# Optimization experiments

Hardware: AMD Instinct MI355X
Metric: run time of the kernel (lower is better)

## Reference

```python
import jax, jax.numpy as jnp
import numpy as np

V = 10000          # vocab_size
D = 64             # gnn_hidden_dim
L = 8              # tokens per node/edge
DG = 256           # gpt_hidden_dim
NH = 4             # attention heads
N_NODES = 8192
N_EDGES = 2048
PAD = 0
MASK_ID = 4
SPECIAL = jnp.array([0, 1, 2, 3], dtype=jnp.int32)


def setup_inputs() -> dict:
    key = jax.random.key(0)
    ks = jax.random.split(key, 20)
    node_tokens = jax.random.randint(ks[0], (N_NODES, L), 0, V, dtype=jnp.int32)
    edge_tokens = jax.random.randint(ks[1], (N_EDGES, L), 0, V, dtype=jnp.int32)
    edge_index = jax.random.randint(ks[2], (2, N_EDGES), 0, N_NODES, dtype=jnp.int32)
    mask_rows = jax.random.bernoulli(ks[3], 0.15, (N_EDGES,))

    def rn(k, shp, scale):
        return (jax.random.normal(k, shp, jnp.float32) * scale).astype(jnp.float32)

    FD = L * D  # flattened per-node feature dim = 512
    emb = rn(ks[4], (V, D), 0.02).at[PAD].set(0.0)  # padding_idx row zeroed
    W_msg = rn(ks[5], (FD, FD), FD ** -0.5)
    W_node = rn(ks[6], (FD, FD), FD ** -0.5)
    lc1_w = rn(ks[7], (D, DG), D ** -0.5)
    lc1_b = jnp.zeros((DG,), jnp.float32)
    lc2_w = rn(ks[8], (DG, D), DG ** -0.5)
    lc2_b = jnp.zeros((D,), jnp.float32)
    Wq = rn(ks[9], (DG, DG), DG ** -0.5)
    Wk = rn(ks[10], (DG, DG), DG ** -0.5)
    Wv = rn(ks[11], (DG, DG), DG ** -0.5)
    Wo = rn(ks[12], (DG, DG), DG ** -0.5)
    Wf1 = rn(ks[13], (DG, 4 * DG), DG ** -0.5)
    Wf2 = rn(ks[14], (4 * DG, DG), (4 * DG) ** -0.5)
    return {
        "node_tokens": node_tokens, "edge_tokens": edge_tokens,
        "edge_index": edge_index, "mask_rows": mask_rows,
        "emb": emb, "W_msg": W_msg, "W_node": W_node,
        "lc1_w": lc1_w, "lc1_b": lc1_b, "lc2_w": lc2_w, "lc2_b": lc2_b,
        "Wq": Wq, "Wk": Wk, "Wv": Wv, "Wo": Wo, "Wf1": Wf1, "Wf2": Wf2,
    }


def _transformer(x, Wq, Wk, Wv, Wo, Wf1, Wf2):
    # single attention + FFN block; returns hidden states (text_summary[1])
    B, S, Dm = x.shape
    hd = Dm // NH
    q = (x @ Wq).reshape(B, S, NH, hd)
    k = (x @ Wk).reshape(B, S, NH, hd)
    v = (x @ Wv).reshape(B, S, NH, hd)
    att = jnp.einsum('bqhd,bkhd->bhqk', q, k) / jnp.sqrt(jnp.float32(hd))
    a = jax.nn.softmax(att, axis=-1)
    o = jnp.einsum('bhqk,bkhd->bqhd', a, v).reshape(B, S, Dm) @ Wo
    x = x + o
    x = x + jax.nn.gelu(x @ Wf1) @ Wf2
    return x


def reference(node_tokens, edge_tokens, edge_index, mask_rows,
              emb, W_msg, W_node, lc1_w, lc1_b, lc2_w, lc2_b,
              Wq, Wk, Wv, Wo, Wf1, Wf2):
    # --- MLM-style edge-token masking (mask_label with masked_edge=True) ---
    special_ok = ~jnp.isin(edge_tokens, SPECIAL)        # get_special_tokens_mask
    masked_idx = mask_rows[:, None] & special_ok        # [E, L]
    labels = jnp.where(masked_idx, edge_tokens, -100)
    m_tokens = jnp.where(masked_idx, MASK_ID, edge_tokens)

    # --- per-row embedding lookup (vectorized) + flatten to [N, L*D] ---
    x = emb[node_tokens].reshape(N_NODES, L * D)
    e = emb[m_tokens].reshape(N_EDGES, L * D)

    # --- GNN message passing: edge message + scatter-add to dst nodes ---
    src, dst = edge_index[0], edge_index[1]
    msg = jax.nn.relu(e @ W_msg + x[src])               # [E, L*D]
    agg = jax.ops.segment_sum(msg, dst, num_segments=N_NODES)
    h = jax.nn.relu(x @ W_node + agg)                   # [N, L*D]

    # --- edge-index gather-add: embeddings[src] + embeddings[dst] ---
    eh = h[src] + h[dst]                                # [E, L*D]
    z = eh.reshape(N_EDGES, L, D)

    # --- liner_connection_1 -> transformer -> liner_connection_2 ---
    z = z @ lc1_w + lc1_b                               # [E, L, DG]
    hs = _transformer(z, Wq, Wk, Wv, Wo, Wf1, Wf2)
    y = hs @ lc2_w + lc2_b                              # [E, L, D]

    # --- tied lm_head + softmax ---
    logits = y @ emb.T                                  # [E, L, V]
    probs = jax.nn.softmax(logits, axis=-1)
    return labels, probs
```

## Files before the change

### kernel.cpp

```cpp
#include <hip/hip_runtime.h>
#include <math.h>

#define VOCAB 10000
#define DIM 64
#define LTOK 8
#define DGPT 256
#define NHEAD 4
#define NNODES 8192
#define NEDGES 2048
#define FDIM 512
#define NROWS (NEDGES*LTOK)

__global__ __launch_bounds__(256) void k_mask(const int* __restrict__ etok,
                                              const int* __restrict__ mrows,
                                              float* __restrict__ labels,
                                              int* __restrict__ mtok) {
    int i = blockIdx.x * 256 + threadIdx.x;
    int e = i >> 3;
    int t = etok[i];
    bool m = (mrows[e] != 0) && (t > 3);
    labels[i] = m ? (float)t : -100.0f;
    mtok[i] = m ? 4 : t;
}

__global__ __launch_bounds__(256) void k_embed(const int* __restrict__ tok,
                                               const float* __restrict__ emb,
                                               float* __restrict__ outf, int total) {
    int i = blockIdx.x * 256 + threadIdx.x;
    if (i >= total) return;
    int d = i & 63;
    int tl = i >> 6;
    outf[i] = emb[(size_t)tok[tl] * DIM + d];
}

__global__ __launch_bounds__(256) void k_eh(const float* __restrict__ h,
                                            const int* __restrict__ src,
                                            const int* __restrict__ dst,
                                            float* __restrict__ eh) {
    int i = blockIdx.x * 256 + threadIdx.x;
    int e = i >> 9; int f = i & 511;
    eh[i] = h[(size_t)src[e] * FDIM + f] + h[(size_t)dst[e] * FDIM + f];
}

__global__ __launch_bounds__(256) void gemm_kernel(
    const float* __restrict__ A, const float* __restrict__ W,
    const float* __restrict__ bias, const float* __restrict__ res,
    const int* __restrict__ resIdx, const int* __restrict__ dstIdx,
    float* __restrict__ out, int M, int N, int K, int act)
{
    __shared__ float As[16][68];
    __shared__ float Ws[16][68];
    int tid = threadIdx.x;
    int row0 = blockIdx.x * 64, col0 = blockIdx.y * 64;
    int ty = tid >> 4, tx = tid & 15;
    float acc[4][4] = {};
    int arow = tid >> 2;
    int acol4 = (tid & 3) * 4;
    int wrow = tid >> 4;
    int wcol4 = (tid & 15) * 4;

    for (int kc = 0; kc < K; kc += 16) {
        float4 av = *(const float4*)&A[(size_t)(row0 + arow) * K + kc + acol4];
        float4 wv = *(const float4*)&W[(size_t)(kc + wrow) * N + col0 + wcol4];
        __syncthreads();
        As[acol4 + 0][arow] = av.x;
        As[acol4 + 1][arow] = av.y;
        As[acol4 + 2][arow] = av.z;
        As[acol4 + 3][arow] = av.w;
        *(float4*)&Ws[wrow][wcol4] = wv;
        __syncthreads();
#pragma unroll
        for (int kk = 0; kk < 16; kk++) {
            float4 a4 = *(const float4*)&As[kk][ty * 4];
            float4 w4 = *(const float4*)&Ws[kk][tx * 4];
            float ar[4] = {a4.x, a4.y, a4.z, a4.w};
            float wr[4] = {w4.x, w4.y, w4.z, w4.w};
#pragma unroll
            for (int i = 0; i < 4; i++)
#pragma unroll
                for (int j = 0; j < 4; j++)
                    acc[i][j] += ar[i] * wr[j];
        }
    }

    const float c0 = 0.7978845608028654f, c1 = 0.044715f;
#pragma unroll
    for (int i = 0; i < 4; i++) {
        int row = row0 + ty * 4 + i;
        int rrow = resIdx ? resIdx[row] : row;
#pragma unroll
        for (int j = 0; j < 4; j++) {
            int col = col0 + tx * 4 + j;
            float v = acc[i][j];
            if (bias) v += bias[col];
            if (res)  v += res[(size_t)rrow * N + col];
            if (act == 1) v = fmaxf(v, 0.0f);
            else if (act == 2) { float t = v; v = 0.5f * t * (1.0f + tanhf(c0 * (t + c1 * t * t * t))); }
            if (dstIdx) atomicAdd(&out[(size_t)dstIdx[row] * N + col], v);
            else out[(size_t)row * N + col] = v;
        }
    }
}

__global__ __launch_bounds__(256) void k_attn(const float* __restrict__ q,
                                              const float* __restrict__ k,
                                              const float* __restrict__ v,
                                              float* __restrict__ o) {
    __shared__ float qs[8 * 256], ks[8 * 256], vs[8 * 256];
    __shared__ float sc[4 * 8 * 8];
    int b = blockIdx.x, t = threadIdx.x;
    const size_t base = (size_t)b * (8 * 256);
    for (int i = t; i < 2048; i += 256) { qs[i] = q[base + i]; ks[i] = k[base + i]; vs[i] = v[base + i]; }
    __syncthreads();
    {
        int h = t >> 6, sq = (t >> 3) & 7, sk = t & 7;
        float acc = 0.0f;
#pragma unroll
        for (int d = 0; d < 64; d++) acc += qs[sq * 256 + h * 64 + d] * ks[sk * 256 + h * 64 + d];
        sc[t] = acc * 0.125f;
    }
    __syncthreads();
    if (t < 32) {
        int h = t >> 3, sq = t & 7;
        float* r = &sc[h * 64 + sq * 8];
        float M = r[0];
        for (int i = 1; i < 8; i++) M = fmaxf(M, r[i]);
        float S = 0.0f, ex[8];
        for (int i = 0; i < 8; i++) { ex[i] = __expf(r[i] - M); S += ex[i]; }
        float inv = 1.0f / S;
        for (int i = 0; i < 8; i++) r[i] = ex[i] * inv;
    }
    __syncthreads();
    {
        int col = t; int h = col >> 6;
#pragma unroll
        for (int sq = 0; sq < 8; sq++) {
            float a = 0.0f;
#pragma unroll
            for (int sk = 0; sk < 8; sk++) a += sc[h * 64 + sq * 8 + sk] * vs[sk * 256 + col];
            o[base + sq * 256 + col] = a;
        }
    }
}

__global__ __launch_bounds__(256) void k_logits(const float* __restrict__ Y,
                                                const float* __restrict__ emb,
                                                float* __restrict__ probs) {
    __shared__ float ys[128][64];
    int t = threadIdx.x;
    int v = blockIdx.y * 256 + t;
    bool vok = v < VOCAB;

    float er[64];
    {
        const float4* ep = (const float4*)&emb[(size_t)(vok ? v : 0) * DIM];
#pragma unroll
        for (int i = 0; i < 16; i++) {
            float4 e4 = ep[i];
            er[4*i+0] = e4.x; er[4*i+1] = e4.y; er[4*i+2] = e4.z; er[4*i+3] = e4.w;
        }
    }

    int r0 = blockIdx.x * 512;
    for (int c = 0; c < 512; c += 128) {
        __syncthreads();
#pragma unroll
        for (int q = 0; q < 8; q++) {
            int fidx = q * 256 + t;
            int row = fidx >> 4;
            int k4 = (fidx & 15) * 4;
            *(float4*)&ys[row][k4] = *(const float4*)&Y[(size_t)(r0 + c + row) * DIM + k4];
        }
        __syncthreads();

        for (int r = 0; r < 128; r += 4) {
            float a0 = 0.f, a1 = 0.f, a2 = 0.f, a3 = 0.f;
#pragma unroll
            for (int kk = 0; kk < 16; kk++) {
                float4 y0 = *(const float4*)&ys[r + 0][kk * 4];
                float4 y1 = *(const float4*)&ys[r + 1][kk * 4];
                float4 y2 = *(const float4*)&ys[r + 2][kk * 4];
                float4 y3 = *(const float4*)&ys[r + 3][kk * 4];
                float e0 = er[4*kk+0], e1 = er[4*kk+1], e2 = er[4*kk+2], e3 = er[4*kk+3];
                a0 += y0.x * e0; a0 += y0.y * e1; a0 += y0.z * e2; a0 += y0.w * e3;
                a1 += y1.x * e0; a1 += y1.y * e1; a1 += y1.z * e2; a1 += y1.w * e3;
                a2 += y2.x * e0; a2 += y2.y * e1; a2 += y2.z * e2; a2 += y2.w * e3;
                a3 += y3.x * e0; a3 += y3.y * e1; a3 += y3.z * e2; a3 += y3.w * e3;
            }
            if (vok) {
                size_t base = (size_t)(r0 + c + r) * VOCAB + v;
                probs[base]             = a0;
                probs[base +     VOCAB] = a1;
                probs[base + 2 * VOCAB] = a2;
                probs[base + 3 * VOCAB] = a3;
            }
        }
    }
}

__global__ __launch_bounds__(256) void k_softmax(float* __restrict__ probs) {
    __shared__ float4 sdata[VOCAB / 4];
    __shared__ float wred[8];
    int t = threadIdx.x;
    float4* prow = (float4*)&probs[(size_t)blockIdx.x * VOCAB];

    float m = -1e30f;
#pragma unroll
    for (int i = 0; i < 10; i++) {
        int j = t + 256 * i;
        if (j < VOCAB / 4) {
            float4 v4 = prow[j];
            sdata[j] = v4;
            m = fmaxf(fmaxf(fmaxf(m, v4.x), v4.y), fmaxf(v4.z, v4.w));
        }
    }
#pragma unroll
    for (int off = 32; off; off >>= 1) m = fmaxf(m, __shfl_xor(m, off, 64));
    if ((t & 63) == 0) wred[t >> 6] = m;
    __syncthreads();
    float M = fmaxf(fmaxf(wred[0], wred[1]), fmaxf(wred[2], wred[3]));

    float s = 0.0f;
#pragma unroll
    for (int i = 0; i < 10; i++) {
        int j = t + 256 * i;
        if (j < VOCAB / 4) {
            float4 v4 = sdata[j];
            v4.x = __expf(v4.x - M); v4.y = __expf(v4.y - M);
            v4.z = __expf(v4.z - M); v4.w = __expf(v4.w - M);
            sdata[j] = v4;
            s += v4.x + v4.y + v4.z + v4.w;
        }
    }
#pragma unroll
    for (int off = 32; off; off >>= 1) s += __shfl_xor(s, off, 64);
    if ((t & 63) == 0) wred[4 + (t >> 6)] = s;
    __syncthreads();
    float Sinv = 1.0f / (wred[4] + wred[5] + wred[6] + wred[7]);

#pragma unroll
    for (int i = 0; i < 10; i++) {
        int j = t + 256 * i;
        if (j < VOCAB / 4) {
            float4 v4 = sdata[j];
            v4.x *= Sinv; v4.y *= Sinv; v4.z *= Sinv; v4.w *= Sinv;
            prow[j] = v4;
        }
    }
}

extern "C" void kernel_launch(void* const* d_in, const int* in_sizes, int n_in,
                              void* d_out, int out_size, void* d_ws, size_t ws_size,
                              hipStream_t stream) {
    const int* node_tokens = (const int*)d_in[0];
    const int* edge_tokens = (const int*)d_in[1];
    const int* edge_index  = (const int*)d_in[2];
    const int* mask_rows   = (const int*)d_in[3];
    const float* emb    = (const float*)d_in[4];
    const float* W_msg  = (const float*)d_in[5];
    const float* W_node = (const float*)d_in[6];
    const float* lc1_w  = (const float*)d_in[7];
    const float* lc1_b  = (const float*)d_in[8];
    const float* lc2_w  = (const float*)d_in[9];
    const float* lc2_b  = (const float*)d_in[10];
    const float* Wq     = (const float*)d_in[11];
    const float* Wk     = (const float*)d_in[12];
    const float* Wv     = (const float*)d_in[13];
    const float* Wo     = (const float*)d_in[14];
    const float* Wf1    = (const float*)d_in[15];
    const float* Wf2    = (const float*)d_in[16];

    const int* src = edge_index;
    const int* dst = edge_index + NEDGES;

    float* labels = (float*)d_out;
    float* probs  = labels + NROWS;

    float* ws = (float*)d_ws;
    float* X   = ws;
    float* E_  = X   + 4194304;
    float* AGG = E_  + 1048576;
    float* EH  = AGG + 4194304;
    float* Z1  = EH  + 1048576;
    float* Q_  = Z1  + 4194304;
    float* K_  = Q_  + 4194304;
    float* Vv  = K_  + 4194304;
    float* O_  = Vv  + 4194304;
    float* X2  = O_  + 4194304;
    float* U_  = X2  + 4194304;
    float* Y2  = U_  + 16777216;
    float* Y_  = Y2  + 4194304;
    int*  MTOK = (int*)(Y_ + 1048576);

    hipMemsetAsync(AGG, 0, (size_t)NNODES * FDIM * sizeof(float), stream);

    k_mask<<<NROWS / 256, 256, 0, stream>>>(edge_tokens, mask_rows, labels, MTOK);

    k_embed<<<(NNODES * FDIM) / 256, 256, 0, stream>>>(node_tokens, emb, X, NNODES * FDIM);
    k_embed<<<(NEDGES * FDIM) / 256, 256, 0, stream>>>(MTOK, emb, E_, NEDGES * FDIM);

    gemm_kernel<<<dim3(NEDGES / 64, FDIM / 64), 256, 0, stream>>>(
        E_, W_msg, nullptr, X, src, dst, AGG, NEDGES, FDIM, FDIM, 1);

    gemm_kernel<<<dim3(NNODES / 64, FDIM / 64), 256, 0, stream>>>(
        X, W_node, nullptr, AGG, nullptr, nullptr, AGG, NNODES, FDIM, FDIM, 1);

    k_eh<<<(NEDGES * FDIM) / 256, 256, 0, stream>>>(AGG, src, dst, EH);

    gemm_kernel<<<dim3(NROWS / 64, DGPT / 64), 256, 0, stream>>>(
        EH, lc1_w, lc1_b, nullptr, nullptr, nullptr, Z1, NROWS, DGPT, DIM, 0);

    gemm_kernel<<<dim3(NROWS / 64, DGPT / 64), 256, 0, stream>>>(
        Z1, Wq, nullptr, nullptr, nullptr, nullptr, Q_, NROWS, DGPT, DGPT, 0);
    gemm_kernel<<<dim3(NROWS / 64, DGPT / 64), 256, 0, stream>>>(
        Z1, Wk, nullptr, nullptr, nullptr, nullptr, K_, NROWS, DGPT, DGPT, 0);
    gemm_kernel<<<dim3(NROWS / 64, DGPT / 64), 256, 0, stream>>>(
        Z1, Wv, nullptr, nullptr, nullptr, nullptr, Vv, NROWS, DGPT, DGPT, 0);

    k_attn<<<NEDGES, 256, 0, stream>>>(Q_, K_, Vv, O_);

    gemm_kernel<<<dim3(NROWS / 64, DGPT / 64), 256, 0, stream>>>(
        O_, Wo, nullptr, Z1, nullptr, nullptr, X2, NROWS, DGPT, DGPT, 0);

    gemm_kernel<<<dim3(NROWS / 64, (4 * DGPT) / 64), 256, 0, stream>>>(
        X2, Wf1, nullptr, nullptr, nullptr, nullptr, U_, NROWS, 4 * DGPT, DGPT, 2);

    gemm_kernel<<<dim3(NROWS / 64, DGPT / 64), 256, 0, stream>>>(
        U_, Wf2, nullptr, X2, nullptr, nullptr, Y2, NROWS, DGPT, 4 * DGPT, 0);

    gemm_kernel<<<dim3(NROWS / 64, DIM / 64), 256, 0, stream>>>(
        Y2, lc2_w, lc2_b, nullptr, nullptr, nullptr, Y_, NROWS, DIM, DGPT, 0);

    k_logits<<<dim3(NROWS / 512, (VOCAB + 255) / 256), 256, 0, stream>>>(Y_, emb, probs);
    k_softmax<<<NROWS, 256, 0, stream>>>(probs);
}
```

Before: 1.777 ms.

## Add 128x128 register-tiled GEMM for large matmuls and widen logits tile

Adds a 128x128-tile GEMM with 8x8 per-thread register blocking and a transposed A tile in shared memory. It replaces the 64-tile GEMM for the node update and both FFN matmuls. The logits kernel now computes two vocab columns per thread over 256 rows instead of one column over 512 rows, reusing each shared Y load twice. The aim is higher arithmetic intensity and fewer shared and global loads per FLOP, at the cost of more registers and lower occupancy. The vocab-0 column is assumed always in range.

```diff
diff --git a/kernel.cpp b/kernel.cpp
--- a/kernel.cpp
+++ b/kernel.cpp
@@ -102,6 +102,78 @@
     }
 }
 
+__global__ __launch_bounds__(256, 3) void gemm128(
+    const float* __restrict__ A, const float* __restrict__ W,
+    const float* __restrict__ bias, const float* __restrict__ res,
+    float* __restrict__ out, int M, int N, int K, int act)
+{
+    __shared__ float As[16][132];
+    __shared__ float Ws[16][132];
+    int tid = threadIdx.x;
+    int row0 = blockIdx.x * 128, col0 = blockIdx.y * 128;
+    int ty = tid >> 4, tx = tid & 15;
+    float acc[8][8] = {};
+
+    for (int kc = 0; kc < K; kc += 16) {
+        float4 av[2], wv[2];
+#pragma unroll
+        for (int q = 0; q < 2; q++) {
+            int fidx = q * 256 + tid;
+            int arow = fidx >> 2;
+            int ak4  = (fidx & 3) * 4;
+            av[q] = *(const float4*)&A[(size_t)(row0 + arow) * K + kc + ak4];
+            int wrow = fidx >> 5;
+            int wc4  = (fidx & 31) * 4;
+            wv[q] = *(const float4*)&W[(size_t)(kc + wrow) * N + col0 + wc4];
+        }
+        __syncthreads();
+#pragma unroll
+        for (int q = 0; q < 2; q++) {
+            int fidx = q * 256 + tid;
+            int arow = fidx >> 2;
+            int ak4  = (fidx & 3) * 4;
+            As[ak4 + 0][arow] = av[q].x;
+            As[ak4 + 1][arow] = av[q].y;
+            As[ak4 + 2][arow] = av[q].z;
+            As[ak4 + 3][arow] = av[q].w;
+            int wrow = fidx >> 5;
+            int wc4  = (fidx & 31) * 4;
+            *(float4*)&Ws[wrow][wc4] = wv[q];
+        }
+        __syncthreads();
+#pragma unroll
+        for (int kk = 0; kk < 16; kk++) {
+            float4 aA = *(const float4*)&As[kk][ty * 4];
+            float4 aB = *(const float4*)&As[kk][64 + ty * 4];
+            float4 wA = *(const float4*)&Ws[kk][tx * 4];
+            float4 wB = *(const float4*)&Ws[kk][64 + tx * 4];
+            float ar[8] = {aA.x, aA.y, aA.z, aA.w, aB.x, aB.y, aB.z, aB.w};
+            float wr[8] = {wA.x, wA.y, wA.z, wA.w, wB.x, wB.y, wB.z, wB.w};
+#pragma unroll
+            for (int i = 0; i < 8; i++)
+#pragma unroll
+                for (int j = 0; j < 8; j++)
+                    acc[i][j] += ar[i] * wr[j];
+        }
+    }
+
+    const float c0 = 0.7978845608028654f, c1 = 0.044715f;
+#pragma unroll
+    for (int i = 0; i < 8; i++) {
+        int row = row0 + (i < 4 ? ty * 4 + i : 64 + ty * 4 + (i - 4));
+#pragma unroll
+        for (int j = 0; j < 8; j++) {
+            int col = col0 + (j < 4 ? tx * 4 + j : 64 + tx * 4 + (j - 4));
+            float v = acc[i][j];
+            if (bias) v += bias[col];
+            if (res)  v += res[(size_t)row * N + col];
+            if (act == 1) v = fmaxf(v, 0.0f);
+            else if (act == 2) { float t = v; v = 0.5f * t * (1.0f + tanhf(c0 * (t + c1 * t * t * t))); }
+            out[(size_t)row * N + col] = v;
+        }
+    }
+}
+
 __global__ __launch_bounds__(256) void k_attn(const float* __restrict__ q,
                                               const float* __restrict__ k,
                                               const float* __restrict__ v,
@@ -143,26 +215,29 @@
     }
 }
 
-__global__ __launch_bounds__(256) void k_logits(const float* __restrict__ Y,
-                                                const float* __restrict__ emb,
-                                                float* __restrict__ probs) {
+__global__ __launch_bounds__(256, 3) void k_logits(const float* __restrict__ Y,
+                                                   const float* __restrict__ emb,
+                                                   float* __restrict__ probs) {
     __shared__ float ys[128][64];
     int t = threadIdx.x;
-    int v = blockIdx.y * 256 + t;
-    bool vok = v < VOCAB;
-
-    float er[64];
+    int v0 = blockIdx.y * 512 + t;
+    int v1 = v0 + 256;
+    bool v1ok = v1 < VOCAB;
+
+    float er0[64], er1[64];
     {
-        const float4* ep = (const float4*)&emb[(size_t)(vok ? v : 0) * DIM];
+        const float4* ep0 = (const float4*)&emb[(size_t)v0 * DIM];
+        const float4* ep1 = (const float4*)&emb[(size_t)(v1ok ? v1 : 0) * DIM];
 #pragma unroll
         for (int i = 0; i < 16; i++) {
-            float4 e4 = ep[i];
-            er[4*i+0] = e4.x; er[4*i+1] = e4.y; er[4*i+2] = e4.z; er[4*i+3] = e4.w;
-        }
-    }
-
-    int r0 = blockIdx.x * 512;
-    for (int c = 0; c < 512; c += 128) {
+            float4 a = ep0[i], b = ep1[i];
+            er0[4*i+0] = a.x; er0[4*i+1] = a.y; er0[4*i+2] = a.z; er0[4*i+3] = a.w;
+            er1[4*i+0] = b.x; er1[4*i+1] = b.y; er1[4*i+2] = b.z; er1[4*i+3] = b.w;
+        }
+    }
+
+    int r0 = blockIdx.x * 256;
+    for (int c = 0; c < 256; c += 128) {
         __syncthreads();
 #pragma unroll
         for (int q = 0; q < 8; q++) {
@@ -174,25 +249,35 @@
         __syncthreads();
 
         for (int r = 0; r < 128; r += 4) {
-            float a0 = 0.f, a1 = 0.f, a2 = 0.f, a3 = 0.f;
+            float a00 = 0.f, a10 = 0.f, a20 = 0.f, a30 = 0.f;
+            float a01 = 0.f, a11 = 0.f, a21 = 0.f, a31 = 0.f;
 #pragma unroll
             for (int kk = 0; kk < 16; kk++) {
                 float4 y0 = *(const float4*)&ys[r + 0][kk * 4];
                 float4 y1 = *(const float4*)&ys[r + 1][kk * 4];
                 float4 y2 = *(const float4*)&ys[r + 2][kk * 4];
                 float4 y3 = *(const float4*)&ys[r + 3][kk * 4];
-                float e0 = er[4*kk+0], e1 = er[4*kk+1], e2 = er[4*kk+2], e3 = er[4*kk+3];
-                a0 += y0.x * e0; a0 += y0.y * e1; a0 += y0.z * e2; a0 += y0.w * e3;
-                a1 += y1.x * e0; a1 += y1.y * e1; a1 += y1.z * e2; a1 += y1.w * e3;
-                a2 += y2.x * e0; a2 += y2.y * e1; a2 += y2.z * e2; a2 += y2.w * e3;
-                a3 += y3.x * e0; a3 += y3.y * e1; a3 += y3.z * e2; a3 += y3.w * e3;
+                float e0 = er0[4*kk+0], e1 = er0[4*kk+1], e2 = er0[4*kk+2], e3 = er0[4*kk+3];
+                float f0 = er1[4*kk+0], f1 = er1[4*kk+1], f2 = er1[4*kk+2], f3 = er1[4*kk+3];
+                a00 += y0.x * e0; a00 += y0.y * e1; a00 += y0.z * e2; a00 += y0.w * e3;
+                a10 += y1.x * e0; a10 += y1.y * e1; a10 += y1.z * e2; a10 += y1.w * e3;
+                a20 += y2.x * e0; a20 += y2.y * e1; a20 += y2.z * e2; a20 += y2.w * e3;
+                a30 += y3.x * e0; a30 += y3.y * e1; a30 += y3.z * e2; a30 += y3.w * e3;
+                a01 += y0.x * f0; a01 += y0.y * f1; a01 += y0.z * f2; a01 += y0.w * f3;
+                a11 += y1.x * f0; a11 += y1.y * f1; a11 += y1.z * f2; a11 += y1.w * f3;
+                a21 += y2.x * f0; a21 += y2.y * f1; a21 += y2.z * f2; a21 += y2.w * f3;
+                a31 += y3.x * f0; a31 += y3.y * f1; a31 += y3.z * f2; a31 += y3.w * f3;
             }
-            if (vok) {
-                size_t base = (size_t)(r0 + c + r) * VOCAB + v;
-                probs[base]             = a0;
-                probs[base +     VOCAB] = a1;
-                probs[base + 2 * VOCAB] = a2;
-                probs[base + 3 * VOCAB] = a3;
+            size_t base = (size_t)(r0 + c + r) * VOCAB;
+            probs[base             + v0] = a00;
+            probs[base +     VOCAB + v0] = a10;
+            probs[base + 2 * VOCAB + v0] = a20;
+            probs[base + 3 * VOCAB + v0] = a30;
+            if (v1ok) {
+                probs[base             + v1] = a01;
+                probs[base +     VOCAB + v1] = a11;
+                probs[base + 2 * VOCAB + v1] = a21;
+                probs[base + 3 * VOCAB + v1] = a31;
             }
         }
     }
@@ -302,8 +387,8 @@
     gemm_kernel<<<dim3(NEDGES / 64, FDIM / 64), 256, 0, stream>>>(
         E_, W_msg, nullptr, X, src, dst, AGG, NEDGES, FDIM, FDIM, 1);
 
-    gemm_kernel<<<dim3(NNODES / 64, FDIM / 64), 256, 0, stream>>>(
-        X, W_node, nullptr, AGG, nullptr, nullptr, AGG, NNODES, FDIM, FDIM, 1);
+    gemm128<<<dim3(NNODES / 128, FDIM / 128), 256, 0, stream>>>(
+        X, W_node, nullptr, AGG, AGG, NNODES, FDIM, FDIM, 1);
 
     k_eh<<<(NEDGES * FDIM) / 256, 256, 0, stream>>>(AGG, src, dst, EH);
 
@@ -322,15 +407,15 @@
     gemm_kernel<<<dim3(NROWS / 64, DGPT / 64), 256, 0, stream>>>(
         O_, Wo, nullptr, Z1, nullptr, nullptr, X2, NROWS, DGPT, DGPT, 0);
 
-    gemm_kernel<<<dim3(NROWS / 64, (4 * DGPT) / 64), 256, 0, stream>>>(
-        X2, Wf1, nullptr, nullptr, nullptr, nullptr, U_, NROWS, 4 * DGPT, DGPT, 2);
-
-    gemm_kernel<<<dim3(NROWS / 64, DGPT / 64), 256, 0, stream>>>(
-        U_, Wf2, nullptr, X2, nullptr, nullptr, Y2, NROWS, DGPT, 4 * DGPT, 0);
+    gemm128<<<dim3(NROWS / 128, (4 * DGPT) / 128), 256, 0, stream>>>(
+        X2, Wf1, nullptr, nullptr, U_, NROWS, 4 * DGPT, DGPT, 2);
+
+    gemm128<<<dim3(NROWS / 128, DGPT / 128), 256, 0, stream>>>(
+        U_, Wf2, nullptr, X2, Y2, NROWS, DGPT, 4 * DGPT, 0);
 
     gemm_kernel<<<dim3(NROWS / 64, DIM / 64), 256, 0, stream>>>(
         Y2, lc2_w, lc2_b, nullptr, nullptr, nullptr, Y_, NROWS, DIM, DGPT, 0);
 
-    k_logits<<<dim3(NROWS / 512, (VOCAB + 255) / 256), 256, 0, stream>>>(Y_, emb, probs);
+    k_logits<<<dim3(NROWS / 256, (VOCAB + 511) / 512), 256, 0, stream>>>(Y_, emb, probs);
     k_softmax<<<NROWS, 256, 0, stream>>>(probs);
 }
```

Result: slower. 5.945 ms (+234.6%).
